# Kernel optimization log

Hardware: AMD Instinct MI355X
Metric: run time of the kernel (lower is better)

Reference implementation:

```python
import jax, jax.numpy as jnp
import numpy as np

B, T = 64, 512
V, F, H = 30000, 256, 256
K = 32          # type_num
PAD, START, END = 0, 30, 31


def make_transition():
    # replicate the exact init order of the torch code
    t = jnp.zeros((K, K), jnp.float32)
    t = t.at[:, START].set(-10000.0)
    t = t.at[END, :].set(-10000.0)
    t = t.at[:, PAD].set(-10000.0)
    t = t.at[PAD, PAD].set(0.0)
    t = t.at[PAD, :END].set(0.0)
    return t


def setup_inputs() -> dict:
    key = jax.random.key(0)
    ks = jax.random.split(key, 12)
    x = jax.random.randint(ks[0], (B, T), 0, V, dtype=jnp.int32)
    tags = jax.random.randint(ks[1], (B, T), 1, START, dtype=jnp.int32)  # real tags, no pad/start/end
    lengths = jax.random.randint(ks[2], (B,), T // 2, T + 1, dtype=jnp.int32)
    mask = (jnp.arange(T, dtype=jnp.int32)[None, :] < lengths[:, None]).astype(jnp.int32)
    s = 0.05
    emb = jax.random.normal(ks[3], (V, F), jnp.float32) * (2.0 / (V + F)) ** 0.5 * 10  # xavier-ish
    w_ih_f = jax.random.normal(ks[4], (4 * H, F), jnp.float32) * s
    w_hh_f = jax.random.normal(ks[5], (4 * H, H), jnp.float32) * s
    b_f = jax.random.normal(ks[6], (4 * H,), jnp.float32) * s  # = b_ih + b_hh (they only ever sum)
    w_ih_b = jax.random.normal(ks[7], (4 * H, F), jnp.float32) * s
    w_hh_b = jax.random.normal(ks[8], (4 * H, H), jnp.float32) * s
    b_b = jax.random.normal(ks[9], (4 * H,), jnp.float32) * s
    w_fc = jax.random.normal(ks[10], (K, 2 * H), jnp.float32) * s
    b_fc = jax.random.normal(ks[11], (K,), jnp.float32) * s
    transition = make_transition()
    return dict(x=x, tags=tags, mask=mask, emb=emb,
                w_ih_f=w_ih_f, w_hh_f=w_hh_f, b_f=b_f,
                w_ih_b=w_ih_b, w_hh_b=w_hh_b, b_b=b_b,
                w_fc=w_fc, b_fc=b_fc, transition=transition)


def _lstm_scan(gx, w_hh):
    # gx: [T, B, 4H] precomputed input gates; PyTorch gate order i, f, g, o
    h0 = jnp.zeros((gx.shape[1], w_hh.shape[1]), gx.dtype)

    def step(carry, g):
        h, c = carry
        z = g + h @ w_hh.T
        i, f, gg, o = jnp.split(z, 4, axis=-1)
        c = jax.nn.sigmoid(f) * c + jax.nn.sigmoid(i) * jnp.tanh(gg)
        h = jax.nn.sigmoid(o) * jnp.tanh(c)
        return (h, c), h

    _, hs = jax.lax.scan(step, (h0, h0), gx)
    return hs  # [T, B, H]


def _crf_loss(scores, tags, mask, transition):
    # scores: [B, T, K], tags/mask: [B, T]
    maskf = mask.astype(scores.dtype)
    b_idx = jnp.arange(scores.shape[0])

    # ---- true path score ----
    first = transition[START, tags[:, 0]] + scores[b_idx, 0, tags[:, 0]]
    tag_sc = jnp.take_along_axis(scores, tags[..., None].astype(jnp.int32), axis=2)[..., 0]  # [B,T]
    tran_sc = transition[tags[:, :-1], tags[:, 1:]]  # [B,T-1]
    body = jnp.sum((tran_sc + tag_sc[:, 1:]) * maskf[:, 1:], axis=1)
    last_idx = jnp.sum(mask, axis=1) - 1
    last_tag = jnp.take_along_axis(tags, last_idx[:, None], axis=1)[:, 0]
    true_prob = first + body + transition[last_tag, END]

    # ---- partition (forward algorithm) via scan ----
    alpha0 = transition[START][None, :] + scores[:, 0]  # [B,K]

    def step(alpha, inp):
        sc, m = inp  # sc: [B,K], m: [B]
        new = jax.nn.logsumexp(alpha[:, :, None] + transition[None, :, :] + sc[:, None, :], axis=1)
        alpha = jnp.where(m[:, None] > 0, new, alpha)
        return alpha, None

    alpha, _ = jax.lax.scan(step, alpha0,
                            (scores.transpose(1, 0, 2)[1:], mask.T[1:]))
    total_prob = jax.nn.logsumexp(alpha + transition[:, END][None, :], axis=1)
    return -jnp.sum(true_prob - total_prob)


def reference(x, tags, mask, emb, w_ih_f, w_hh_f, b_f, w_ih_b, w_hh_b, b_b, w_fc, b_fc, transition):
    e = emb[x]                       # [B,T,F] embedding lookup (dropout = identity, eval mode)
    xt = e.transpose(1, 0, 2)        # [T,B,F]
    # forward direction
    h_f = _lstm_scan(xt @ w_ih_f.T + b_f, w_hh_f)           # [T,B,H]
    # backward direction: reverse time, scan, reverse back
    h_b = _lstm_scan((xt @ w_ih_b.T + b_b)[::-1], w_hh_b)[::-1]
    h = jnp.concatenate([h_f, h_b], axis=-1).transpose(1, 0, 2)  # [B,T,2H]
    scores = h @ w_fc.T + b_fc       # [B,T,K]
    return _crf_loss(scores, tags, mask, transition)
```

## Files before the change

### kernel.cpp

```cpp
#include <hip/hip_runtime.h>

typedef __attribute__((ext_vector_type(8))) short short8;
typedef __attribute__((ext_vector_type(4))) float floatx4;
typedef __attribute__((ext_vector_type(8))) int int8v;

__device__ __forceinline__ float bf2f(unsigned short u) {
    union { unsigned int i; float f; } c; c.i = ((unsigned int)u) << 16; return c.f;
}
__device__ __forceinline__ unsigned short f2bf(float f) {
    union { float f; unsigned int i; } c; c.f = f;
    unsigned int u = c.i;
    return (unsigned short)((u + 0x7FFFu + ((u >> 16) & 1u)) >> 16);
}
__device__ __forceinline__ unsigned short f2bf_rz(float f) {
    union { float f; unsigned int i; } c; c.f = f;
    return (unsigned short)(c.i >> 16);
}
__device__ __forceinline__ float sigm(float x) {
    return __builtin_amdgcn_rcpf(1.f + __expf(-x));
}
__device__ __forceinline__ float tanh_(float x) {
    return 1.f - 2.f * __builtin_amdgcn_rcpf(1.f + __expf(2.f * x));
}

__device__ __forceinline__ void glds16(const void* g, void* l) {
    __builtin_amdgcn_global_load_lds((const __attribute__((address_space(1))) unsigned int*)g,
                                     (__attribute__((address_space(3))) unsigned int*)l, 16, 0, 0);
}

__global__ void k_cast_weights(const float* __restrict__ wihf, const float* __restrict__ wihb,
                               const float* __restrict__ wfc, unsigned short* __restrict__ dst) {
    int i = blockIdx.x * 256 + threadIdx.x;
    if (i >= 532480) return;
    float v;
    if (i < 262144) v = wihf[i];
    else if (i < 524288) v = wihb[i - 262144];
    else v = wfc[i - 524288];
    dst[i] = f2bf(v);
}

__global__ void k_cast_fp8(const float* __restrict__ whhf, const float* __restrict__ whhb,
                           unsigned char* __restrict__ dst) {
    int i = blockIdx.x * 256 + threadIdx.x;
    if (i >= 262144) return;
    int e = i * 2;
    float a = (e < 262144) ? whhf[e] : whhb[e - 262144];
    float b = (e + 1 < 262144) ? whhf[e + 1] : whhb[e + 1 - 262144];
    int p = __builtin_amdgcn_cvt_pk_fp8_f32(a, b, 0, false);
    *(unsigned short*)(dst + e) = (unsigned short)(p & 0xffff);
}

__global__ void k_gather(const int* __restrict__ x, const float* __restrict__ emb,
                         unsigned short* __restrict__ et) {
    int id = blockIdx.x * 256 + threadIdx.x;
    int m = id >> 5, fi = (id & 31) << 3;
    int b = m & 63, t = m >> 6;
    int v = x[b * 512 + t];
    const float4* s = (const float4*)(emb + ((size_t)v << 8) + fi);
    float4 a = s[0], q = s[1];
    uint4 o;
    o.x = (unsigned)f2bf(a.x) | ((unsigned)f2bf(a.y) << 16);
    o.y = (unsigned)f2bf(a.z) | ((unsigned)f2bf(a.w) << 16);
    o.z = (unsigned)f2bf(q.x) | ((unsigned)f2bf(q.y) << 16);
    o.w = (unsigned)f2bf(q.z) | ((unsigned)f2bf(q.w) << 16);
    *(uint4*)(et + ((size_t)m << 8) + fi) = o;
}

__global__ __launch_bounds__(256, 2) void k_gx(const unsigned short* __restrict__ et,
                                               const unsigned short* __restrict__ wcat,
                                               const float* __restrict__ bfv, const float* __restrict__ bbv,
                                               unsigned short* __restrict__ gx) {
    __shared__ unsigned short As[4096];
    __shared__ unsigned short Bs[4096];
    const int tid = threadIdx.x;
    const int w = tid >> 6, l = tid & 63, quad = l >> 4, col = l & 15;
    const size_t m0 = (size_t)blockIdx.x * 128, n0 = (size_t)blockIdx.y * 128;
    floatx4 C[4][4];
    #pragma unroll
    for (int i = 0; i < 4; ++i)
        #pragma unroll
        for (int j = 0; j < 4; ++j) C[i][j] = (floatx4){0.f, 0.f, 0.f, 0.f};
    const int srow = tid >> 2, scol = (tid & 3) * 16;
    for (int it = 0; it < 8; ++it) {
        const char* ga = (const char*)et + (m0 + srow) * 512 + it * 64 + scol;
        const char* gb = (const char*)wcat + (n0 + srow) * 512 + it * 64 + scol;
        glds16(ga,             (char*)As + w * 1024);
        glds16(ga + 64 * 512,  (char*)As + 4096 + w * 1024);
        glds16(gb,             (char*)Bs + w * 1024);
        glds16(gb + 64 * 512,  (char*)Bs + 4096 + w * 1024);
        __syncthreads();
        short8 Af[4], Bf[4];
        #pragma unroll
        for (int i = 0; i < 4; ++i) {
            Af[i] = *(const short8*)(As + (((w & 1) * 64 + i * 16 + col) * 32 + quad * 8));
            Bf[i] = *(const short8*)(Bs + (((w >> 1) * 64 + i * 16 + col) * 32 + quad * 8));
        }
        #pragma unroll
        for (int i = 0; i < 4; ++i)
            #pragma unroll
            for (int j = 0; j < 4; ++j)
                C[i][j] = __builtin_amdgcn_mfma_f32_16x16x32_bf16(Af[i], Bf[j], C[i][j], 0, 0, 0);
        __syncthreads();
    }
    const int mw = (w & 1) * 64, nw = (w >> 1) * 64;
    #pragma unroll
    for (int j = 0; j < 4; ++j) {
        int n = (int)n0 + nw + j * 16 + col;
        float bias = (n < 1024) ? bfv[n] : bbv[n - 1024];
        size_t dbase = (size_t)(n >> 10) * 33554432 + (size_t)(n & 1023);
        #pragma unroll
        for (int i = 0; i < 4; ++i)
            #pragma unroll
            for (int r = 0; r < 4; ++r) {
                size_t m = m0 + mw + i * 16 + quad * 4 + r;
                gx[dbase + m * 1024] = f2bf(C[i][j][r] + bias);
            }
    }
}

__global__ __launch_bounds__(512, 2) void k_lstm(const unsigned char* __restrict__ w8_all,
                                                 const unsigned short* __restrict__ gx_all,
                                                 unsigned short* __restrict__ hcat) {
    const int d = blockIdx.x >> 5, bg = blockIdx.x & 31;
    const int tid = threadIdx.x, w = tid >> 6, l = tid & 63, quad = l >> 4, col = l & 15;
    const unsigned char* W = w8_all + (size_t)d * 262144;
    const unsigned short* G = gx_all + (size_t)d * 33554432;
    __shared__ __align__(32) unsigned char hld[2][2][288];

    int8v Wb[4][2][2];
    #pragma unroll
    for (int g = 0; g < 4; ++g)
        #pragma unroll
        for (int nt = 0; nt < 2; ++nt)
            #pragma unroll
            for (int kt = 0; kt < 2; ++kt)
                Wb[g][nt][kt] = *(const int8v*)(W + (size_t)(256 * g + 32 * w + 16 * nt + col) * 256
                                                + kt * 128 + quad * 32);
    for (int i = tid; i < 288; i += 512) ((unsigned int*)hld)[i] = 0;

    const int b = l >> 5, u = 32 * w + (l & 31);
    const int bglob = 2 * bg + b;
    const int nts = quad & 1, rs = quad >> 1;
    float cst = 0.f;
    const long gstep = d ? -65536 : 65536;
    const long hstep = d ? -32768 : 32768;
    const unsigned short* gp = G + ((size_t)((d ? 511 : 0) * 64 + bglob) * 1024 + u);
    unsigned short* hp = hcat + ((size_t)((d ? 511 : 0) * 64 + bglob) * 512 + d * 256 + u);
    unsigned short gq0 = gp[0], gq1 = gp[256], gq2 = gp[512], gq3 = gp[768];
    gp += gstep;
    __syncthreads();

    #pragma clang loop unroll(disable)
    for (int step = 0; step < 512; ++step) {
        const int cur = step & 1;
        int8v Af[2];
        #pragma unroll
        for (int kt = 0; kt < 2; ++kt)
            Af[kt] = *(const int8v*)(&hld[cur][col & 1][kt * 128 + quad * 32]);
        floatx4 C[4][2];
        #pragma unroll
        for (int g = 0; g < 4; ++g)
            #pragma unroll
            for (int nt = 0; nt < 2; ++nt) C[g][nt] = (floatx4){0.f, 0.f, 0.f, 0.f};
        #pragma unroll
        for (int kt = 0; kt < 2; ++kt)
            #pragma unroll
            for (int g = 0; g < 4; ++g)
                #pragma unroll
                for (int nt = 0; nt < 2; ++nt)
                    C[g][nt] = __builtin_amdgcn_mfma_scale_f32_16x16x128_f8f6f4(
                        Af[kt], Wb[g][nt][kt], C[g][nt], 0, 0, 0, 0x7f7f7f7f, 0, 0x7f7f7f7f);
        float t0, t1, z0, z1, z2, z3;
        t0 = nts ? C[0][1][0] : C[0][0][0];
        t1 = nts ? C[0][1][1] : C[0][0][1];
        z0 = rs ? t1 : t0;
        t0 = nts ? C[1][1][0] : C[1][0][0];
        t1 = nts ? C[1][1][1] : C[1][0][1];
        z1 = rs ? t1 : t0;
        t0 = nts ? C[2][1][0] : C[2][0][0];
        t1 = nts ? C[2][1][1] : C[2][0][1];
        z2 = rs ? t1 : t0;
        t0 = nts ? C[3][1][0] : C[3][0][0];
        t1 = nts ? C[3][1][1] : C[3][0][1];
        z3 = rs ? t1 : t0;
        float vi = z0 + bf2f(gq0);
        float vf = z1 + bf2f(gq1);
        float vg = z2 + bf2f(gq2);
        float vo = z3 + bf2f(gq3);
        gq0 = gp[0]; gq1 = gp[256]; gq2 = gp[512]; gq3 = gp[768];
        gp += gstep;
        float cc = sigm(vf) * cst + sigm(vi) * tanh_(vg);
        cst = cc;
        float hf = sigm(vo) * tanh_(cc);
        *hp = f2bf_rz(hf);
        hp += hstep;
        int pk = __builtin_amdgcn_cvt_pk_fp8_f32(hf, hf, 0, false);
        hld[cur ^ 1][b][u] = (unsigned char)(pk & 0xff);
        __builtin_amdgcn_sched_barrier(0);
        asm volatile("s_waitcnt lgkmcnt(0)");
        __builtin_amdgcn_sched_barrier(0);
        __builtin_amdgcn_s_barrier();
        __builtin_amdgcn_sched_barrier(0);
    }
}

__global__ __launch_bounds__(256, 4) void k_scores(const unsigned short* __restrict__ hcat,
                                                   const unsigned short* __restrict__ wfc,
                                                   const float* __restrict__ bfc,
                                                   float* __restrict__ sc) {
    const int tid = threadIdx.x, w = tid >> 6, l = tid & 63, quad = l >> 4, col = l & 15;
    const int m0 = blockIdx.x * 64 + w * 16;
    floatx4 C0 = (floatx4){0.f, 0.f, 0.f, 0.f}, C1 = C0;
    #pragma unroll
    for (int kt = 0; kt < 16; ++kt) {
        short8 A  = *(const short8*)(hcat + (size_t)(m0 + col) * 512 + kt * 32 + quad * 8);
        short8 B0 = *(const short8*)(wfc + (size_t)col * 512 + kt * 32 + quad * 8);
        short8 B1 = *(const short8*)(wfc + (size_t)(16 + col) * 512 + kt * 32 + quad * 8);
        C0 = __builtin_amdgcn_mfma_f32_16x16x32_bf16(A, B0, C0, 0, 0, 0);
        C1 = __builtin_amdgcn_mfma_f32_16x16x32_bf16(A, B1, C1, 0, 0, 0);
    }
    float b0 = bfc[col], b1 = bfc[16 + col];
    #pragma unroll
    for (int r = 0; r < 4; ++r) {
        int m = m0 + quad * 4 + r;
        sc[(size_t)m * 32 + col] = C0[r] + b0;
        sc[(size_t)m * 32 + 16 + col] = C1[r] + b1;
    }
}

__global__ __launch_bounds__(1024, 1) void k_crf(const float* __restrict__ sc, const int* __restrict__ tags,
                                                 const int* __restrict__ mask, const float* __restrict__ tr,
                                                 float* __restrict__ out) {
    __shared__ float Tm[32][33];
    __shared__ float al[2][32];
    __shared__ float trueb;
    const int b = blockIdx.x, tid = threadIdx.x;
    { int i = tid >> 5, j = tid & 31; Tm[i][j] = tr[tid]; }
    __syncthreads();
    if (tid < 64) {
        float acc = 0.f; int cnt = 0;
        for (int t = tid; t < 512; t += 64) cnt += mask[b * 512 + t];
        for (int t = tid + 1; t < 512; t += 64) {
            if (mask[b * 512 + t]) {
                int tg = tags[b * 512 + t], tp = tags[b * 512 + t - 1];
                acc += Tm[tp][tg] + sc[((size_t)t * 64 + b) * 32 + tg];
            }
        }
        #pragma unroll
        for (int m = 1; m < 64; m <<= 1) { acc += __shfl_xor(acc, m); cnt += __shfl_xor(cnt, m); }
        if (tid == 0) {
            int tg0 = tags[b * 512];
            float first = Tm[30][tg0] + sc[(size_t)b * 32 + tg0];
            int lt = tags[b * 512 + cnt - 1];
            trueb = first + acc + Tm[lt][31];
        }
    }
    if (tid < 32) al[0][tid] = Tm[30][tid] + sc[(size_t)b * 32 + tid];
    __syncthreads();
    const int j = tid >> 5, i = tid & 31;
    int cur = 0;
    float scn = sc[((size_t)64 + b) * 32 + j];
    int mkn = mask[b * 512 + 1];
    #pragma clang loop unroll(disable)
    for (int t = 1; t < 512; ++t) {
        float v = al[cur][i] + Tm[i][j];
        float mx = v;
        #pragma unroll
        for (int m = 1; m < 32; m <<= 1) mx = fmaxf(mx, __shfl_xor(mx, m));
        float e = __expf(v - mx);
        #pragma unroll
        for (int m = 1; m < 32; m <<= 1) e += __shfl_xor(e, m);
        float nv = mx + __logf(e) + scn;
        int mk = mkn;
        int tn = t < 511 ? t + 1 : 511;
        scn = sc[((size_t)tn * 64 + b) * 32 + j];
        mkn = mask[b * 512 + tn];
        if (i == 0) al[cur ^ 1][j] = mk ? nv : al[cur][j];
        __syncthreads();
        cur ^= 1;
    }
    if (tid < 32) {
        float v = al[cur][tid] + Tm[tid][31];
        float mx = v;
        #pragma unroll
        for (int m = 1; m < 32; m <<= 1) mx = fmaxf(mx, __shfl_xor(mx, m));
        float e = __expf(v - mx);
        #pragma unroll
        for (int m = 1; m < 32; m <<= 1) e += __shfl_xor(e, m);
        if (tid == 0) atomicAdd(out, mx + __logf(e) - trueb);
    }
}

extern "C" void kernel_launch(void* const* d_in, const int* in_sizes, int n_in,
                              void* d_out, int out_size, void* d_ws, size_t ws_size,
                              hipStream_t stream) {
    const int* x      = (const int*)d_in[0];
    const int* tags   = (const int*)d_in[1];
    const int* mask   = (const int*)d_in[2];
    const float* emb  = (const float*)d_in[3];
    const float* wihf = (const float*)d_in[4];
    const float* whhf = (const float*)d_in[5];
    const float* bf_  = (const float*)d_in[6];
    const float* wihb = (const float*)d_in[7];
    const float* whhb = (const float*)d_in[8];
    const float* bb_  = (const float*)d_in[9];
    const float* wfc  = (const float*)d_in[10];
    const float* bfc  = (const float*)d_in[11];
    const float* tr   = (const float*)d_in[12];

    char* ws = (char*)d_ws;
    unsigned short* et   = (unsigned short*)(ws);
    unsigned short* wbf  = (unsigned short*)(ws + 16777216);
    unsigned char*  w8   = (unsigned char*)(ws + 17842176);
    unsigned short* gx   = (unsigned short*)(ws + 18366464);
    unsigned short* hcat = (unsigned short*)(ws + 152584192);
    float* sc            = (float*)(ws + 186138624);

    hipMemsetAsync(d_out, 0, sizeof(float), stream);
    k_cast_weights<<<2080, 256, 0, stream>>>(wihf, wihb, wfc, wbf);
    k_cast_fp8<<<1024, 256, 0, stream>>>(whhf, whhb, w8);
    k_gather<<<4096, 256, 0, stream>>>(x, emb, et);
    dim3 g2(256, 16);
    k_gx<<<g2, 256, 0, stream>>>(et, wbf, bf_, bb_, gx);
    k_lstm<<<64, 512, 0, stream>>>(w8, gx, hcat);
    k_scores<<<512, 256, 0, stream>>>(hcat, wbf + 524288, bfc, sc);
    k_crf<<<64, 1024, 0, stream>>>(sc, tags, mask, tr, (float*)d_out);
}
```

Measured before the change: 917.4 us.

## Interleave gate columns in gx and load all four gates per step with one read

The input-projection GEMM now writes gx with the four gates of each hidden unit interleaved, so the LSTM recurrence can fetch i,f,g,o as one 8-byte load instead of four strided 2-byte loads. The A-fragment row selection is changed so each lane's needed result lands in element 0 of the accumulator. This removes the per-step select chains across rows and lets MFMA chains be ordered per gate. It relies on the GEMM epilogue and the recurrence agreeing on the new interleaved layout, and the GEMM store pattern becomes more scattered.

```diff
diff --git a/kernel.cpp b/kernel.cpp
--- a/kernel.cpp
+++ b/kernel.cpp
@@ -6,6 +6,9 @@
 
 __device__ __forceinline__ float bf2f(unsigned short u) {
     union { unsigned int i; float f; } c; c.i = ((unsigned int)u) << 16; return c.f;
+}
+__device__ __forceinline__ float asf(unsigned int u) {
+    union { unsigned int i; float f; } c; c.i = u; return c.f;
 }
 __device__ __forceinline__ unsigned short f2bf(float f) {
     union { float f; unsigned int i; } c; c.f = f;
@@ -107,7 +110,7 @@
     for (int j = 0; j < 4; ++j) {
         int n = (int)n0 + nw + j * 16 + col;
         float bias = (n < 1024) ? bfv[n] : bbv[n - 1024];
-        size_t dbase = (size_t)(n >> 10) * 33554432 + (size_t)(n & 1023);
+        size_t dbase = (size_t)(n >> 10) * 33554432 + (size_t)(((n & 255) << 2) | ((n >> 8) & 3));
         #pragma unroll
         for (int i = 0; i < 4; ++i)
             #pragma unroll
@@ -125,7 +128,7 @@
     const int tid = threadIdx.x, w = tid >> 6, l = tid & 63, quad = l >> 4, col = l & 15;
     const unsigned char* W = w8_all + (size_t)d * 262144;
     const unsigned short* G = gx_all + (size_t)d * 33554432;
-    __shared__ __align__(32) unsigned char hld[2][2][288];
+    __shared__ __align__(16) unsigned char hld[2][2][288];
 
     int8v Wb[4][2][2];
     #pragma unroll
@@ -140,13 +143,14 @@
 
     const int b = l >> 5, u = 32 * w + (l & 31);
     const int bglob = 2 * bg + b;
-    const int nts = quad & 1, rs = quad >> 1;
+    const int nts = quad & 1;
+    const int hsel = (l >> 3) & 1;
     float cst = 0.f;
     const long gstep = d ? -65536 : 65536;
     const long hstep = d ? -32768 : 32768;
-    const unsigned short* gp = G + ((size_t)((d ? 511 : 0) * 64 + bglob) * 1024 + u);
+    const unsigned short* gp = G + ((size_t)((d ? 511 : 0) * 64 + bglob) * 1024 + u * 4);
     unsigned short* hp = hcat + ((size_t)((d ? 511 : 0) * 64 + bglob) * 512 + d * 256 + u);
-    unsigned short gq0 = gp[0], gq1 = gp[256], gq2 = gp[512], gq3 = gp[768];
+    uint2 gq = *(const uint2*)gp;
     gp += gstep;
     __syncthreads();
 
@@ -156,38 +160,26 @@
         int8v Af[2];
         #pragma unroll
         for (int kt = 0; kt < 2; ++kt)
-            Af[kt] = *(const int8v*)(&hld[cur][col & 1][kt * 128 + quad * 32]);
-        floatx4 C[4][2];
-        #pragma unroll
-        for (int g = 0; g < 4; ++g)
+            Af[kt] = *(const int8v*)(&hld[cur][hsel][kt * 128 + quad * 32]);
+        float z[4];
+        #pragma unroll
+        for (int g = 0; g < 4; ++g) {
+            floatx4 c0 = (floatx4){0.f, 0.f, 0.f, 0.f};
+            floatx4 c1 = (floatx4){0.f, 0.f, 0.f, 0.f};
             #pragma unroll
-            for (int nt = 0; nt < 2; ++nt) C[g][nt] = (floatx4){0.f, 0.f, 0.f, 0.f};
-        #pragma unroll
-        for (int kt = 0; kt < 2; ++kt)
-            #pragma unroll
-            for (int g = 0; g < 4; ++g)
-                #pragma unroll
-                for (int nt = 0; nt < 2; ++nt)
-                    C[g][nt] = __builtin_amdgcn_mfma_scale_f32_16x16x128_f8f6f4(
-                        Af[kt], Wb[g][nt][kt], C[g][nt], 0, 0, 0, 0x7f7f7f7f, 0, 0x7f7f7f7f);
-        float t0, t1, z0, z1, z2, z3;
-        t0 = nts ? C[0][1][0] : C[0][0][0];
-        t1 = nts ? C[0][1][1] : C[0][0][1];
-        z0 = rs ? t1 : t0;
-        t0 = nts ? C[1][1][0] : C[1][0][0];
-        t1 = nts ? C[1][1][1] : C[1][0][1];
-        z1 = rs ? t1 : t0;
-        t0 = nts ? C[2][1][0] : C[2][0][0];
-        t1 = nts ? C[2][1][1] : C[2][0][1];
-        z2 = rs ? t1 : t0;
-        t0 = nts ? C[3][1][0] : C[3][0][0];
-        t1 = nts ? C[3][1][1] : C[3][0][1];
-        z3 = rs ? t1 : t0;
-        float vi = z0 + bf2f(gq0);
-        float vf = z1 + bf2f(gq1);
-        float vg = z2 + bf2f(gq2);
-        float vo = z3 + bf2f(gq3);
-        gq0 = gp[0]; gq1 = gp[256]; gq2 = gp[512]; gq3 = gp[768];
+            for (int kt = 0; kt < 2; ++kt) {
+                c0 = __builtin_amdgcn_mfma_scale_f32_16x16x128_f8f6f4(
+                    Af[kt], Wb[g][0][kt], c0, 0, 0, 0, 0x7f7f7f7f, 0, 0x7f7f7f7f);
+                c1 = __builtin_amdgcn_mfma_scale_f32_16x16x128_f8f6f4(
+                    Af[kt], Wb[g][1][kt], c1, 0, 0, 0, 0x7f7f7f7f, 0, 0x7f7f7f7f);
+            }
+            z[g] = nts ? c1[0] : c0[0];
+        }
+        float vi = z[0] + asf(gq.x << 16);
+        float vf = z[1] + asf(gq.x & 0xffff0000u);
+        float vg = z[2] + asf(gq.y << 16);
+        float vo = z[3] + asf(gq.y & 0xffff0000u);
+        gq = *(const uint2*)gp;
         gp += gstep;
         float cc = sigm(vf) * cst + sigm(vi) * tanh_(vg);
         cst = cc;
```

New measurement: 961.9 us. +4.9%, slower.
